# Performance work log

Measured on AMD Instinct MI355X. Metric: run time of the kernel, lower is better.

## Reference

```python
import jax, jax.numpy as jnp
import numpy as np

N_RAYS = 524288
N_PTS = 64            # coarse samples per ray (last dim of lengths)
N_FINE = 64           # n_pts_per_ray (fine samples drawn from the pdf)
EPS = 1e-5


def setup_inputs() -> dict:
    key = jax.random.key(0)
    k1, k2, k3, k4, k5 = jax.random.split(key, 5)
    origins = jax.random.normal(k1, (N_RAYS, 3), dtype=jnp.float32)
    directions = jax.random.normal(k2, (N_RAYS, 3), dtype=jnp.float32)
    # lengths are monotonically increasing depths along each ray (near ~2.0)
    deltas = jax.random.uniform(k3, (N_RAYS, N_PTS), dtype=jnp.float32, minval=0.01, maxval=0.1)
    lengths = 2.0 + jnp.cumsum(deltas, axis=-1)
    xys = jax.random.uniform(k4, (N_RAYS, 2), dtype=jnp.float32)
    ray_weights = jax.random.uniform(k5, (N_RAYS, N_PTS), dtype=jnp.float32)
    return {"origins": origins, "directions": directions, "lengths": lengths,
            "xys": xys, "ray_weights": ray_weights}


def _sample_pdf_det(bins, weights, n_samples, eps):
    # bins: [R, n_bins+1], weights: [R, n_bins]; deterministic (det=True) sampling
    weights = weights + eps
    pdf = weights / jnp.sum(weights, axis=-1, keepdims=True)
    cdf = jnp.cumsum(pdf, axis=-1)
    cdf = jnp.concatenate([jnp.zeros_like(cdf[..., :1]), cdf], axis=-1)  # [R, n_bins+1]
    u = jnp.linspace(0.0, 1.0, n_samples, dtype=cdf.dtype)
    u = jnp.broadcast_to(u, cdf.shape[:-1] + (n_samples,))               # [R, n_samples]
    # batched searchsorted (right): per-ray binary search
    inds = jax.vmap(lambda c, uu: jnp.searchsorted(c, uu, side='right'))(cdf, u)
    below = jnp.maximum(inds - 1, 0)
    above = jnp.minimum(inds, cdf.shape[-1] - 1)
    cdf_b = jnp.take_along_axis(cdf, below, axis=-1)
    cdf_a = jnp.take_along_axis(cdf, above, axis=-1)
    bins_b = jnp.take_along_axis(bins, below, axis=-1)
    bins_a = jnp.take_along_axis(bins, above, axis=-1)
    denom = cdf_a - cdf_b
    denom = jnp.where(denom < eps, jnp.ones_like(denom), denom)
    t = (u - cdf_b) / denom
    return bins_b + t * (bins_a - bins_b)


def reference(origins, directions, lengths, xys, ray_weights):
    # RayPointRefiner.forward: returns the refined, sorted lengths.
    # (origins/directions/xys pass through unchanged in the original RayBundle.)
    z_vals = lengths                                              # [R, N_PTS]
    # torch.lerp(z[1:], z[:-1], 0.5) == midpoints of adjacent samples
    z_vals_mid = 0.5 * (z_vals[..., 1:] + z_vals[..., :-1])       # [R, N_PTS-1]
    w = ray_weights[..., 1:-1]                                    # [R, N_PTS-2]
    z_samples = _sample_pdf_det(z_vals_mid, w, N_FINE, EPS)       # [R, N_FINE]
    z_samples = jax.lax.stop_gradient(z_samples)                  # torch.no_grad block
    z_all = jnp.concatenate([z_vals, z_samples], axis=-1)         # add_input_samples=True
    z_all = jnp.sort(z_all, axis=-1)                              # [R, N_PTS + N_FINE]
    return z_all
```

## Files before the change

### kernel.cpp

```cpp
#include <hip/hip_runtime.h>

#define N_PTS  64
#define N_FINE 64
#define EPS    1e-5f
#define WAVES_PER_BLOCK 4

__global__ __launch_bounds__(256) void ray_refine_kernel(
    const float* __restrict__ lengths,
    const float* __restrict__ ray_weights,
    float* __restrict__ out,
    int n_rays)
{
    const int lane = threadIdx.x & 63;
    const int wid  = threadIdx.x >> 6;
    int ray = blockIdx.x * WAVES_PER_BLOCK + wid;
    if (ray >= n_rays) ray = n_rays - 1;

    __shared__ float s_cdf[WAVES_PER_BLOCK][64];
    __shared__ float s_mid[WAVES_PER_BLOCK][64];
    __shared__ float s_a[WAVES_PER_BLOCK][64];
    __shared__ float s_b[WAVES_PER_BLOCK][64];
    __shared__ float s_out[WAVES_PER_BLOCK][128];

    const size_t base = (size_t)ray * 64;
    const float z  = lengths[base + lane];
    const float wf = ray_weights[base + lane];

    const float zn  = __shfl_down(z, 1);
    const float mid = 0.5f * (z + zn);

    const float wnext = __shfl_down(wf, 1);
    float w = (lane < 62) ? (wnext + EPS) : 0.0f;

    float c = w;
    #pragma unroll
    for (int off = 1; off < 64; off <<= 1) {
        float y = __shfl_up(c, off);
        if (lane >= off) c += y;
    }
    const float total = __shfl(c, 63);
    const float inv_total = 1.0f / total;

    float* cdf  = s_cdf[wid];
    float* mids = s_mid[wid];
    if (lane < 62) cdf[lane + 1] = c * inv_total;
    if (lane == 63) cdf[0] = 0.0f;
    if (lane < 63) mids[lane] = mid;
    __syncthreads();

    const float u = (lane == 63) ? 1.0f : (float)lane * (1.0f / 63.0f);

    int ind = 0;
    #pragma unroll
    for (int step = 32; step > 0; step >>= 1) {
        int nxt = ind + step;
        if (nxt <= 63 && cdf[nxt - 1] <= u) ind = nxt;
    }
    const int below = (ind - 1 > 0) ? (ind - 1) : 0;
    const int above = (ind < 62) ? ind : 62;
    const float cb = cdf[below];
    const float ca = cdf[above];
    const float bb = mids[below];
    const float ba = mids[above];
    float denom = ca - cb;
    if (denom < EPS) denom = 1.0f;
    const float t = (u - cb) / denom;
    const float sample = bb + t * (ba - bb);

    float* A = s_a[wid];
    float* B = s_b[wid];
    A[lane] = z;
    B[lane] = sample;
    __syncthreads();

    int cntB = 0;
    #pragma unroll
    for (int step = 64; step > 0; step >>= 1) {
        int nxt = cntB + step;
        if (nxt <= 64 && B[nxt - 1] < z) cntB = nxt;
    }
    int cntA = 0;
    #pragma unroll
    for (int step = 64; step > 0; step >>= 1) {
        int nxt = cntA + step;
        if (nxt <= 64 && A[nxt - 1] <= sample) cntA = nxt;
    }

    float* O = s_out[wid];
    O[lane + cntB] = z;
    O[lane + cntA] = sample;
    __syncthreads();

    float2 v;
    v.x = O[2 * lane];
    v.y = O[2 * lane + 1];
    ((float2*)(out + (size_t)ray * 128))[lane] = v;
}

extern "C" void kernel_launch(void* const* d_in, const int* in_sizes, int n_in,
                              void* d_out, int out_size, void* d_ws, size_t ws_size,
                              hipStream_t stream) {
    const float* lengths     = (const float*)d_in[2];
    const float* ray_weights = (const float*)d_in[4];
    float* out = (float*)d_out;

    const int n_rays = in_sizes[2] / N_PTS;
    const int grid = (n_rays + WAVES_PER_BLOCK - 1) / WAVES_PER_BLOCK;
    ray_refine_kernel<<<grid, 256, 0, stream>>>(lengths, ray_weights, out, n_rays);
}
```

Before: 522.2 us.

## Replace binary searches with scatter-and-max-scan using DPP wave scans

Replaces the shuffle-based prefix sum with DPP row scans plus readlane combination. The per-sample binary search over the CDF and the merge-path binary searches are replaced by inverting the uniform grid from each CDF value, scattering indices with LDS atomicMax, and recovering positions with a wave max-scan. The sample's rank is taken from its known bin. Block-wide barriers are removed in favour of an lgkmcnt wait, and output is scattered directly to global memory rather than staged through shared memory. This trades memory-coalesced float2 stores for scattered stores, and relies on wave-local LDS ordering without barriers plus float rounding in the grid inversion.

```diff
diff --git a/kernel.cpp b/kernel.cpp
--- a/kernel.cpp
+++ b/kernel.cpp
@@ -1,9 +1,61 @@
 #include <hip/hip_runtime.h>
 
-#define N_PTS  64
-#define N_FINE 64
-#define EPS    1e-5f
-#define WAVES_PER_BLOCK 4
+#define EPS 1e-5f
+#define WPB 4
+
+template<int CTRL>
+__device__ __forceinline__ float dppf(float v) {
+    return __int_as_float(__builtin_amdgcn_update_dpp(
+        0, __float_as_int(v), CTRL, 0xf, 0xf, true));
+}
+template<int CTRL>
+__device__ __forceinline__ int dppi(int v) {
+    return __builtin_amdgcn_update_dpp(0, v, CTRL, 0xf, 0xf, true);
+}
+
+__device__ __forceinline__ float readlane_f(float v, int l) {
+    return __int_as_float(__builtin_amdgcn_readlane(__float_as_int(v), l));
+}
+
+__device__ __forceinline__ void lds_fence() {
+    asm volatile("s_waitcnt lgkmcnt(0)" ::: "memory");
+}
+
+__device__ __forceinline__ float wave_scan_sum(float x, int lane) {
+    x += dppf<0x111>(x);
+    x += dppf<0x112>(x);
+    x += dppf<0x114>(x);
+    x += dppf<0x118>(x);
+    float r0 = readlane_f(x, 15);
+    float r1 = readlane_f(x, 31);
+    float r2 = readlane_f(x, 47);
+    int row = lane >> 4;
+    float off = 0.0f;
+    if (row == 1) off = r0;
+    else if (row == 2) off = r0 + r1;
+    else if (row == 3) off = (r0 + r1) + r2;
+    return x + off;
+}
+
+__device__ __forceinline__ int wave_scan_max(int x, int lane) {
+    x = max(x, dppi<0x111>(x));
+    x = max(x, dppi<0x112>(x));
+    x = max(x, dppi<0x114>(x));
+    x = max(x, dppi<0x118>(x));
+    int r0 = __builtin_amdgcn_readlane(x, 15);
+    int r1 = __builtin_amdgcn_readlane(x, 31);
+    int r2 = __builtin_amdgcn_readlane(x, 47);
+    int row = lane >> 4;
+    int off = 0;
+    if (row == 1) off = r0;
+    else if (row == 2) off = max(r0, r1);
+    else if (row == 3) off = max(max(r0, r1), r2);
+    return max(x, off);
+}
+
+__device__ __forceinline__ float uval(int j) {
+    return (j >= 63) ? 1.0f : (float)j * (1.0f / 63.0f);
+}
 
 __global__ __launch_bounds__(256) void ray_refine_kernel(
     const float* __restrict__ lengths,
@@ -13,88 +65,65 @@
 {
     const int lane = threadIdx.x & 63;
     const int wid  = threadIdx.x >> 6;
-    int ray = blockIdx.x * WAVES_PER_BLOCK + wid;
+    int ray = blockIdx.x * WPB + wid;
     if (ray >= n_rays) ray = n_rays - 1;
 
-    __shared__ float s_cdf[WAVES_PER_BLOCK][64];
-    __shared__ float s_mid[WAVES_PER_BLOCK][64];
-    __shared__ float s_a[WAVES_PER_BLOCK][64];
-    __shared__ float s_b[WAVES_PER_BLOCK][64];
-    __shared__ float s_out[WAVES_PER_BLOCK][128];
+    __shared__ float sZ[WPB][64];
+    __shared__ float sC[WPB][64];
+    __shared__ int   sS[WPB][64][2];
 
     const size_t base = (size_t)ray * 64;
     const float z  = lengths[base + lane];
     const float wf = ray_weights[base + lane];
 
-    const float zn  = __shfl_down(z, 1);
-    const float mid = 0.5f * (z + zn);
+    float win = (lane >= 1 && lane <= 62) ? (wf + EPS) : 0.0f;
+    float x = wave_scan_sum(win, lane);
+    const float total = readlane_f(x, 62);
+    const float inv_total = 1.0f / total;
+    const float cv = x * inv_total;
 
-    const float wnext = __shfl_down(wf, 1);
-    float w = (lane < 62) ? (wnext + EPS) : 0.0f;
+    sZ[wid][lane] = z;
+    sC[wid][lane] = cv;
+    sS[wid][lane][0] = 0;
+    sS[wid][lane][1] = 0;
+    lds_fence();
 
-    float c = w;
-    #pragma unroll
-    for (int off = 1; off < 64; off <<= 1) {
-        float y = __shfl_up(c, off);
-        if (lane >= off) c += y;
-    }
-    const float total = __shfl(c, 63);
-    const float inv_total = 1.0f / total;
+    int m = (int)ceilf(cv * 63.0f);
+    m = min(max(m, 0), 64);
+    if (m > 0 && cv <= uval(m - 1)) m--;
+    if (m > 0 && cv <= uval(m - 1)) m--;
+    if (m < 64 && cv > uval(m)) m++;
+    if (m < 64 && cv > uval(m)) m++;
+    if (lane < 63 && m < 64) atomicMax(&sS[wid][m][0], lane + 1);
+    lds_fence();
 
-    float* cdf  = s_cdf[wid];
-    float* mids = s_mid[wid];
-    if (lane < 62) cdf[lane + 1] = c * inv_total;
-    if (lane == 63) cdf[0] = 0.0f;
-    if (lane < 63) mids[lane] = mid;
-    __syncthreads();
+    const int ind = wave_scan_max(sS[wid][lane][0], lane);
+    const int below = ind - 1;
+    const int above = min(ind, 62);
 
-    const float u = (lane == 63) ? 1.0f : (float)lane * (1.0f / 63.0f);
-
-    int ind = 0;
-    #pragma unroll
-    for (int step = 32; step > 0; step >>= 1) {
-        int nxt = ind + step;
-        if (nxt <= 63 && cdf[nxt - 1] <= u) ind = nxt;
-    }
-    const int below = (ind - 1 > 0) ? (ind - 1) : 0;
-    const int above = (ind < 62) ? ind : 62;
-    const float cb = cdf[below];
-    const float ca = cdf[above];
-    const float bb = mids[below];
-    const float ba = mids[above];
+    const float cb  = sC[wid][below];
+    const float ca  = sC[wid][above];
+    const float zb  = sZ[wid][below];
+    const float zb1 = sZ[wid][below + 1];
+    const float za  = sZ[wid][above];
+    const float za1 = sZ[wid][above + 1];
+    const float bb = 0.5f * (zb + zb1);
+    const float ba = 0.5f * (za + za1);
     float denom = ca - cb;
     if (denom < EPS) denom = 1.0f;
+    const float u = uval(lane);
     const float t = (u - cb) / denom;
-    const float sample = bb + t * (ba - bb);
+    const float s = bb + t * (ba - bb);
 
-    float* A = s_a[wid];
-    float* B = s_b[wid];
-    A[lane] = z;
-    B[lane] = sample;
-    __syncthreads();
+    const int r = below + 1 + ((above > below && zb1 <= s) ? 1 : 0);
 
-    int cntB = 0;
-    #pragma unroll
-    for (int step = 64; step > 0; step >>= 1) {
-        int nxt = cntB + step;
-        if (nxt <= 64 && B[nxt - 1] < z) cntB = nxt;
-    }
-    int cntA = 0;
-    #pragma unroll
-    for (int step = 64; step > 0; step >>= 1) {
-        int nxt = cntA + step;
-        if (nxt <= 64 && A[nxt - 1] <= sample) cntA = nxt;
-    }
+    atomicMax(&sS[wid][r][1], lane + 1);
+    lds_fence();
+    const int cntB = wave_scan_max(sS[wid][lane][1], lane);
 
-    float* O = s_out[wid];
-    O[lane + cntB] = z;
-    O[lane + cntA] = sample;
-    __syncthreads();
-
-    float2 v;
-    v.x = O[2 * lane];
-    v.y = O[2 * lane + 1];
-    ((float2*)(out + (size_t)ray * 128))[lane] = v;
+    const size_t ob = (size_t)ray * 128;
+    out[ob + lane + cntB] = z;
+    out[ob + lane + r]    = s;
 }
 
 extern "C" void kernel_launch(void* const* d_in, const int* in_sizes, int n_in,
@@ -104,7 +133,7 @@
     const float* ray_weights = (const float*)d_in[4];
     float* out = (float*)d_out;
 
-    const int n_rays = in_sizes[2] / N_PTS;
-    const int grid = (n_rays + WAVES_PER_BLOCK - 1) / WAVES_PER_BLOCK;
+    const int n_rays = in_sizes[2] / 64;
+    const int grid = (n_rays + WPB - 1) / WPB;
     ray_refine_kernel<<<grid, 256, 0, stream>>>(lengths, ray_weights, out, n_rays);
 }
```

Measured after the change: 474.5 us. -9.1%, faster.
